# Performance work log

Measured on AMD Instinct MI355X. Metric: run time of the kernel, lower is better.

The kernel has to match this reference:

```python
import jax, jax.numpy as jnp
import numpy as np
from math import factorial

P = 3          # polynomial order
D_I = 4096     # sketch output dim per order
C = 512        # input channels
B, H, W = 8, 28, 28
GAMMA = 1e-4


def setup_inputs() -> dict:
    key = jax.random.key(0)
    k1, k2, k3 = jax.random.split(key, 3)
    x = jax.random.normal(k1, (B, H, W, C), dtype=jnp.float32)
    # AlphaInitializer: alpha_i = sqrt(exp(-2g) * (2g)^i / i!)
    gam2 = np.full(P + 1, 2.0 * GAMMA)
    numer = np.power(gam2, np.arange(P + 1))
    denom = np.array([factorial(i) for i in range(P + 1)], dtype=np.float64)
    alpha = jnp.asarray(np.sqrt(np.exp(-gam2) * numer / denom), dtype=jnp.float32)
    # count-sketch hash indices and sign bits, one pair per order t in [0, p)
    h_idx = jax.random.randint(k2, (P, C), 0, D_I)
    s_bits = jax.random.randint(k3, (P, C), 0, 2).astype(jnp.int32)
    return {"x": x, "alpha": alpha, "h_idx": h_idx, "s_bits": s_bits}


def reference(x, alpha, h_idx, s_bits):
    Bs, Hs, Ws, Ch = x.shape
    p = h_idx.shape[0]
    d_i = D_I
    signs = (2 * s_bits - 1).astype(x.dtype)          # (p, C) in {-1,+1}
    x_flat = x.reshape(-1, Ch)                        # (B*H*W, C)

    def count_sketch(h, s):
        # scatter-add channels into d_i buckets: equivalent to x_flat @ S
        return jnp.zeros((x_flat.shape[0], d_i), x.dtype).at[:, h].add(x_flat * s)

    sk = jax.vmap(count_sketch)(h_idx, signs)         # (p, N, d_i)
    xs = jnp.transpose(sk, (1, 0, 2)).reshape(Bs, Hs * Ws, p, d_i)

    xf = jnp.fft.fft(xs.astype(jnp.complex64), axis=-1)
    cp = jnp.cumprod(xf, axis=-2)[:, :, 1:, :]        # orders 2..p
    xi = jnp.real(jnp.fft.ifft(cp, axis=-1)).mean(axis=1)   # (B, p-1, d_i)

    x_p = xi * alpha[2:].reshape(1, p - 1, 1)
    zeroth = alpha[0] * jnp.ones((Bs, 1), x.dtype)
    first = alpha[1] * x.mean(axis=(1, 2))            # (B, C)
    phi = jnp.concatenate([zeroth, first, x_p.reshape(Bs, -1)], axis=-1)
    phi = jnp.sign(phi) * jnp.sqrt(jnp.abs(phi) + 1e-12)    # signed sqrt
    return phi / jnp.linalg.norm(phi, axis=-1, keepdims=True)
```

## Files before the change

kernel.cpp:

```cpp
#include <hip/hip_runtime.h>

#define BATCH 8
#define NPOS 784
#define CH 512
#define DI 4096
#define PPC 4
#define CHUNKS (NPOS / PPC)
#define PHI_LEN 8705
#define S_FLOATS (BATCH * 2 * 2049 * 2)
#define PHI_OFF S_FLOATS

__device__ __forceinline__ float2 cmul(float2 a, float2 b) {
  return make_float2(a.x * b.x - a.y * b.y, a.x * b.y + a.y * b.x);
}
__device__ __forceinline__ float2 f2add(float2 a, float2 b) {
  return make_float2(a.x + b.x, a.y + b.y);
}
__device__ __forceinline__ float2 f2sub(float2 a, float2 b) {
  return make_float2(a.x - b.x, a.y - b.y);
}

__device__ __forceinline__ void dft4(float2& a, float2& b, float2& c, float2& d) {
  float t0x = a.x + c.x, t0y = a.y + c.y;
  float t1x = a.x - c.x, t1y = a.y - c.y;
  float t2x = b.x + d.x, t2y = b.y + d.y;
  float t3x = b.x - d.x, t3y = b.y - d.y;
  a = make_float2(t0x + t2x, t0y + t2y);
  c = make_float2(t0x - t2x, t0y - t2y);
  b = make_float2(t1x + t3y, t1y - t3x);
  d = make_float2(t1x - t3y, t1y + t3x);
}

__device__ __forceinline__ void dft8(float2 v[8]) {
  float2 e0 = v[0], e1 = v[2], e2 = v[4], e3 = v[6];
  dft4(e0, e1, e2, e3);
  float2 o0 = v[1], o1 = v[3], o2 = v[5], o3 = v[7];
  dft4(o0, o1, o2, o3);
  const float r = 0.70710678118654752f;
  o1 = make_float2(r * (o1.x + o1.y), r * (o1.y - o1.x));
  o2 = make_float2(o2.y, -o2.x);
  o3 = make_float2(r * (o3.y - o3.x), -r * (o3.x + o3.y));
  v[0] = f2add(e0, o0); v[4] = f2sub(e0, o0);
  v[1] = f2add(e1, o1); v[5] = f2sub(e1, o1);
  v[2] = f2add(e2, o2); v[6] = f2sub(e2, o2);
  v[3] = f2add(e3, o3); v[7] = f2sub(e3, o3);
}

__device__ __forceinline__ void twiddle8(float2 v[8], float2 w) {
  float2 w2 = cmul(w, w);
  float2 w3 = cmul(w2, w);
  float2 w4 = cmul(w2, w2);
  v[1] = cmul(v[1], w);
  v[2] = cmul(v[2], w2);
  v[3] = cmul(v[3], w3);
  v[4] = cmul(v[4], w4);
  v[5] = cmul(v[5], cmul(w4, w));
  v[6] = cmul(v[6], cmul(w4, w2));
  v[7] = cmul(v[7], cmul(w4, w3));
}

__device__ __forceinline__ void fft_stages8(float2* Z, int t, float2 w1b,
                                            float2 w2b, float2 w3b) {
  __syncthreads();
  {
    const int base = t << 3;
    const int mask0 = (t >> 1) & 15;
    float2 v[8];
    #pragma unroll
    for (int u = 0; u < 8; ++u) v[u] = Z[(base + u) ^ mask0];
    dft8(v);
    #pragma unroll
    for (int k = 0; k < 8; ++k) Z[(base + k) ^ mask0] = v[k];
  }
  __builtin_amdgcn_wave_barrier();
  {
    const int base = ((t >> 3) << 6) + (t & 7);
    const int g4 = (t >> 3) << 2;
    float2 v[8];
    #pragma unroll
    for (int u = 0; u < 8; ++u)
      v[u] = Z[(base + (u << 3)) ^ ((g4 + (u >> 1)) & 15)];
    twiddle8(v, w1b);
    dft8(v);
    #pragma unroll
    for (int k = 0; k < 8; ++k)
      Z[(base + (k << 3)) ^ ((g4 + (k >> 1)) & 15)] = v[k];
  }
  __builtin_amdgcn_wave_barrier();
  {
    const int base = ((t >> 6) << 9) + (t & 63);
    const int jh = (t & 63) >> 4;
    float2 v[8];
    #pragma unroll
    for (int u = 0; u < 8; ++u)
      v[u] = Z[(base + (u << 6)) ^ (((u << 2) + jh) & 15)];
    twiddle8(v, w2b);
    dft8(v);
    #pragma unroll
    for (int k = 0; k < 8; ++k)
      Z[(base + (k << 6)) ^ (((k << 2) + jh) & 15)] = v[k];
  }
  __syncthreads();
  {
    const int mask3 = (t >> 4) & 15;
    float2 v[8];
    #pragma unroll
    for (int u = 0; u < 8; ++u) v[u] = Z[(t + (u << 9)) ^ mask3];
    twiddle8(v, w3b);
    dft8(v);
    #pragma unroll
    for (int k = 0; k < 8; ++k) Z[(t + (k << 9)) ^ mask3] = v[k];
  }
  __syncthreads();
}

__global__ __launch_bounds__(512) void cbp_stage1(
    const float* __restrict__ x, const float* __restrict__ alpha,
    const int* __restrict__ h_idx, const int* __restrict__ s_bits,
    float* __restrict__ ws) {
  __shared__ float2 Z[DI];
  float* Zf = (float*)Z;
  const int t = threadIdx.x;
  const int bb = blockIdx.x / CHUNKS;
  const int ch = blockIdx.x % CHUNKS;

  auto mapq = [](int h, int s) {
    int r = ((h & 7) << 9) | (((h >> 3) & 7) << 6) | (((h >> 6) & 7) << 3) |
            (h >> 9);
    return (r ^ ((r >> 4) & 15)) | ((s ^ 1) << 31);
  };
  auto sgn = [](float v, int p) {
    return __int_as_float(__float_as_int(v) ^ ((unsigned)p & 0x80000000u));
  };
  const int q0 = mapq(h_idx[t], s_bits[t]);
  const int q1 = mapq(h_idx[CH + t], s_bits[CH + t]);
  const int q2 = mapq(h_idx[2 * CH + t], s_bits[2 * CH + t]);

  float sv_, cv_;
  __sincosf(-9.8174770424681038e-2f * (float)(t & 7), &sv_, &cv_);
  const float2 w1b = make_float2(cv_, sv_);
  __sincosf(-1.2271846303085130e-2f * (float)(t & 63), &sv_, &cv_);
  const float2 w2b = make_float2(cv_, sv_);
  __sincosf(-1.5339807878856412e-3f * (float)t, &sv_, &cv_);
  const float2 w3b = make_float2(cv_, sv_);

  const int mask3 = (t >> 4) & 15;

  float2 acc2[4], acc3[4], carry[4];
  #pragma unroll
  for (int j = 0; j < 4; ++j) {
    acc2[j] = make_float2(0.f, 0.f);
    acc3[j] = make_float2(0.f, 0.f);
  }
  float acc2x = 0.f, acc3x = 0.f, carryx = 0.f;
  float xs = 0.f;

  #pragma unroll
  for (int q = 0; q < 8; ++q) Z[t + (q << 9)] = make_float2(0.f, 0.f);
  __syncthreads();

  for (int ip = 0; ip < PPC / 2; ++ip) {
    const int n0 = bb * NPOS + ch * PPC + ip * 2;
    const float xv0 = x[(size_t)n0 * CH + t];
    const float xv1 = x[(size_t)(n0 + 1) * CH + t];
    xs += xv0 + xv1;

    atomicAdd(&Zf[2 * (q0 & 0xFFF)], sgn(xv0, q0));
    atomicAdd(&Zf[2 * (q1 & 0xFFF) + 1], sgn(xv0, q1));
    fft_stages8(Z, t, w1b, w2b, w3b);
    #pragma unroll
    for (int jj = 0; jj < 4; ++jj) {
      const int k = t + (jj << 9);
      const int ak = k ^ mask3;
      const int m = (DI - k) & (DI - 1);
      const int am = m ^ ((m >> 4) & 15);
      float2 Zk = Z[ak], Zm = Z[am];
      Z[ak] = make_float2(0.f, 0.f);
      Z[am] = make_float2(0.f, 0.f);
      float2 E = make_float2(0.5f * (Zk.x + Zm.x), 0.5f * (Zk.y - Zm.y));
      float2 O = make_float2(0.5f * (Zk.y + Zm.y), -0.5f * (Zk.x - Zm.x));
      float2 P = cmul(E, O);
      carry[jj] = P;
      acc2[jj].x += P.x;
      acc2[jj].y += P.y;
    }
    if (t == 0) {
      float2 Zq = Z[2048];
      Z[2048] = make_float2(0.f, 0.f);
      carryx = Zq.x * Zq.y;
      acc2x += carryx;
    }
    __syncthreads();

    atomicAdd(&Zf[2 * (q2 & 0xFFF)], sgn(xv0, q2));
    atomicAdd(&Zf[2 * (q0 & 0xFFF) + 1], sgn(xv1, q0));
    fft_stages8(Z, t, w1b, w2b, w3b);
    #pragma unroll
    for (int jj = 0; jj < 4; ++jj) {
      const int k = t + (jj << 9);
      const int ak = k ^ mask3;
      const int m = (DI - k) & (DI - 1);
      const int am = m ^ ((m >> 4) & 15);
      float2 Zk = Z[ak], Zm = Z[am];
      Z[ak] = make_float2(0.f, 0.f);
      Z[am] = make_float2(0.f, 0.f);
      float2 E = make_float2(0.5f * (Zk.x + Zm.x), 0.5f * (Zk.y - Zm.y));
      float2 O = make_float2(0.5f * (Zk.y + Zm.y), -0.5f * (Zk.x - Zm.x));
      float2 P3 = cmul(carry[jj], E);
      acc3[jj].x += P3.x;
      acc3[jj].y += P3.y;
      carry[jj] = O;
    }
    if (t == 0) {
      float2 Zq = Z[2048];
      Z[2048] = make_float2(0.f, 0.f);
      acc3x += carryx * Zq.x;
      carryx = Zq.y;
    }
    __syncthreads();

    atomicAdd(&Zf[2 * (q1 & 0xFFF)], sgn(xv1, q1));
    atomicAdd(&Zf[2 * (q2 & 0xFFF) + 1], sgn(xv1, q2));
    fft_stages8(Z, t, w1b, w2b, w3b);
    #pragma unroll
    for (int jj = 0; jj < 4; ++jj) {
      const int k = t + (jj << 9);
      const int ak = k ^ mask3;
      const int m = (DI - k) & (DI - 1);
      const int am = m ^ ((m >> 4) & 15);
      float2 Zk = Z[ak], Zm = Z[am];
      Z[ak] = make_float2(0.f, 0.f);
      Z[am] = make_float2(0.f, 0.f);
      float2 E = make_float2(0.5f * (Zk.x + Zm.x), 0.5f * (Zk.y - Zm.y));
      float2 O = make_float2(0.5f * (Zk.y + Zm.y), -0.5f * (Zk.x - Zm.x));
      float2 P = cmul(carry[jj], E);
      acc2[jj].x += P.x;
      acc2[jj].y += P.y;
      float2 P3 = cmul(P, O);
      acc3[jj].x += P3.x;
      acc3[jj].y += P3.y;
    }
    if (t == 0) {
      float2 Zq = Z[2048];
      Z[2048] = make_float2(0.f, 0.f);
      float tt = carryx * Zq.x;
      acc2x += tt;
      acc3x += tt * Zq.y;
    }
    __syncthreads();
  }

  float* S = ws;
  #pragma unroll
  for (int jj = 0; jj < 4; ++jj) {
    const int k = t + (jj << 9);
    float* p2p = S + ((size_t)(bb * 2 + 0) * 2049 + k) * 2;
    atomicAdd(p2p, acc2[jj].x);
    atomicAdd(p2p + 1, acc2[jj].y);
    float* p3p = S + ((size_t)(bb * 2 + 1) * 2049 + k) * 2;
    atomicAdd(p3p, acc3[jj].x);
    atomicAdd(p3p + 1, acc3[jj].y);
  }
  if (t == 0) {
    atomicAdd(S + ((size_t)(bb * 2 + 0) * 2049 + 2048) * 2, acc2x);
    atomicAdd(S + ((size_t)(bb * 2 + 1) * 2049 + 2048) * 2, acc3x);
  }

  const float sc1 = alpha[1] * (1.0f / (float)NPOS);
  float* phi = ws + PHI_OFF;
  atomicAdd(&phi[(size_t)bb * PHI_LEN + 1 + t], xs * sc1);
}

__device__ inline void fft4096_r2(float2* Z, const float2* W, int tid) {
  for (int s = 1; s <= 12; ++s) {
    __syncthreads();
    const int half = 1 << (s - 1);
    const int tsh = 12 - s;
    #pragma unroll
    for (int q = 0; q < 8; ++q) {
      int bidx = tid + q * 256;
      int j = bidx & (half - 1);
      int i1 = ((bidx >> (s - 1)) << s) + j;
      int i2 = i1 + half;
      float2 w = W[j << tsh];
      float2 u = Z[i1];
      float2 v = Z[i2];
      float2 t = cmul(w, v);
      Z[i1] = make_float2(u.x + t.x, u.y + t.y);
      Z[i2] = make_float2(u.x - t.x, u.y - t.y);
    }
  }
  __syncthreads();
}

__global__ __launch_bounds__(256) void cbp_stage2(
    const float* __restrict__ ws_in, const float* __restrict__ alpha,
    float* __restrict__ ws_phi) {
  __shared__ float2 Z[DI];
  __shared__ float2 W[DI / 2];
  const int tid = threadIdx.x;

  for (int r = tid; r < DI / 2; r += 256) {
    float ang = 1.5339807878856412e-3f * (float)r;
    float sv, cv;
    sincosf(ang, &sv, &cv);
    W[r] = make_float2(cv, sv);
  }

  const int b = blockIdx.x >> 1;
  const int t = blockIdx.x & 1;
  const float* Sp = ws_in + (size_t)(b * 2 + t) * 2049 * 2;

  for (int k = tid; k <= 2048; k += 256) {
    float re = Sp[k * 2];
    float im = Sp[k * 2 + 1];
    Z[__brev((unsigned)k) >> 20] = make_float2(re, im);
    if (k > 0 && k < 2048) {
      Z[__brev((unsigned)(DI - k)) >> 20] = make_float2(re, -im);
    }
  }
  fft4096_r2(Z, W, tid);

  const float scale = alpha[2 + t] / ((float)DI * (float)NPOS);
  float* out = ws_phi + (size_t)b * PHI_LEN + 513 + t * DI;
  for (int d = tid; d < DI; d += 256) out[d] = Z[d].x * scale;
}

__global__ __launch_bounds__(256) void cbp_stage3(
    const float* __restrict__ ws_phi, const float* __restrict__ alpha,
    float* __restrict__ out) {
  __shared__ float red[4];
  const int b = blockIdx.x;
  const int tid = threadIdx.x;
  const float* pr = ws_phi + (size_t)b * PHI_LEN;
  const float a0 = alpha[0];

  float w[35];
  float ssum = 0.f;
  #pragma unroll
  for (int j = 0; j < 35; ++j) {
    const int idx = tid + j * 256;
    float wv = 0.f;
    if (idx < PHI_LEN) {
      float v = (idx == 0) ? a0 : pr[idx];
      float sq = sqrtf(fabsf(v) + 1e-12f);
      wv = (v > 0.f) ? sq : ((v < 0.f) ? -sq : 0.f);
    }
    w[j] = wv;
    ssum += wv * wv;
  }
  for (int off = 32; off > 0; off >>= 1) ssum += __shfl_down(ssum, off);
  if ((tid & 63) == 0) red[tid >> 6] = ssum;
  __syncthreads();
  const float tot = red[0] + red[1] + red[2] + red[3];
  const float inv = 1.0f / sqrtf(tot);

  #pragma unroll
  for (int j = 0; j < 35; ++j) {
    const int idx = tid + j * 256;
    if (idx < PHI_LEN) out[(size_t)b * PHI_LEN + idx] = w[j] * inv;
  }
}

extern "C" void kernel_launch(void* const* d_in, const int* in_sizes, int n_in,
                              void* d_out, int out_size, void* d_ws,
                              size_t ws_size, hipStream_t stream) {
  const float* x = (const float*)d_in[0];
  const float* alpha = (const float*)d_in[1];
  const int* h_idx = (const int*)d_in[2];
  const int* s_bits = (const int*)d_in[3];
  float* out = (float*)d_out;
  float* ws = (float*)d_ws;

  const size_t zero_bytes = (size_t)(S_FLOATS + BATCH * PHI_LEN) * sizeof(float);
  hipMemsetAsync(d_ws, 0, zero_bytes, stream);

  cbp_stage1<<<dim3(BATCH * CHUNKS), dim3(512), 0, stream>>>(x, alpha, h_idx,
                                                             s_bits, ws);
  cbp_stage2<<<dim3(BATCH * 2), dim3(256), 0, stream>>>(ws, alpha,
                                                        ws + PHI_OFF);
  cbp_stage3<<<dim3(BATCH), dim3(256), 0, stream>>>(ws + PHI_OFF, alpha, out);
}
```

Measured before the change: 224.7 us.

## Fuse last FFT stage with spectral product and replicate global accumulators

The final radix-8 FFT stage is merged with the conjugate-pair spectral product. Threads are remapped so that each k and its mirror 4096-k sit in lanes 32 apart, and the partner value is fetched with a cross-lane shuffle instead of a second shared-memory pass and barrier. Global atomic accumulation of spectra and first-order means is spread over 16 replicated buffers chosen by block index, to reduce atomic contention. Stage 2 and stage 3 then sum the replicas, which adds more memset and read traffic in exchange.

```diff
diff --git a/kernel.cpp b/kernel.cpp
--- a/kernel.cpp
+++ b/kernel.cpp
@@ -7,8 +7,14 @@
 #define PPC 4
 #define CHUNKS (NPOS / PPC)
 #define PHI_LEN 8705
-#define S_FLOATS (BATCH * 2 * 2049 * 2)
-#define PHI_OFF S_FLOATS
+#define REP 16
+#define S_STRIDE (BATCH * 2 * 2049 * 2)
+#define S_FLOATS (REP * S_STRIDE)
+#define FO_OFF S_FLOATS
+#define FO_STRIDE (BATCH * CH)
+#define FO_FLOATS (REP * FO_STRIDE)
+#define PH_OFF (FO_OFF + FO_FLOATS)
+#define ZERO_FLOATS (S_FLOATS + FO_FLOATS)
 
 __device__ __forceinline__ float2 cmul(float2 a, float2 b) {
   return make_float2(a.x * b.x - a.y * b.y, a.x * b.y + a.y * b.x);
@@ -59,59 +65,102 @@
   v[7] = cmul(v[7], cmul(w4, w3));
 }
 
-__device__ __forceinline__ void fft_stages8(float2* Z, int t, float2 w1b,
-                                            float2 w2b, float2 w3b) {
-  __syncthreads();
-  {
-    const int base = t << 3;
-    const int mask0 = (t >> 1) & 15;
-    float2 v[8];
-    #pragma unroll
-    for (int u = 0; u < 8; ++u) v[u] = Z[(base + u) ^ mask0];
-    dft8(v);
-    #pragma unroll
-    for (int k = 0; k < 8; ++k) Z[(base + k) ^ mask0] = v[k];
-  }
-  __builtin_amdgcn_wave_barrier();
-  {
-    const int base = ((t >> 3) << 6) + (t & 7);
-    const int g4 = (t >> 3) << 2;
-    float2 v[8];
-    #pragma unroll
-    for (int u = 0; u < 8; ++u)
-      v[u] = Z[(base + (u << 3)) ^ ((g4 + (u >> 1)) & 15)];
-    twiddle8(v, w1b);
-    dft8(v);
-    #pragma unroll
-    for (int k = 0; k < 8; ++k)
-      Z[(base + (k << 3)) ^ ((g4 + (k >> 1)) & 15)] = v[k];
-  }
-  __builtin_amdgcn_wave_barrier();
-  {
-    const int base = ((t >> 6) << 9) + (t & 63);
-    const int jh = (t & 63) >> 4;
-    float2 v[8];
-    #pragma unroll
-    for (int u = 0; u < 8; ++u)
-      v[u] = Z[(base + (u << 6)) ^ (((u << 2) + jh) & 15)];
-    twiddle8(v, w2b);
-    dft8(v);
-    #pragma unroll
-    for (int k = 0; k < 8; ++k)
-      Z[(base + (k << 6)) ^ (((k << 2) + jh) & 15)] = v[k];
-  }
-  __syncthreads();
-  {
-    const int mask3 = (t >> 4) & 15;
-    float2 v[8];
-    #pragma unroll
-    for (int u = 0; u < 8; ++u) v[u] = Z[(t + (u << 9)) ^ mask3];
-    twiddle8(v, w3b);
-    dft8(v);
-    #pragma unroll
-    for (int k = 0; k < 8; ++k) Z[(t + (k << 9)) ^ mask3] = v[k];
-  }
-  __syncthreads();
+template <int MODE>
+__device__ __forceinline__ void prodpair(float2 Zk, float2 Zm, float2& carry,
+                                         float2& acc2, float2& acc3) {
+  float2 E = make_float2(0.5f * (Zk.x + Zm.x), 0.5f * (Zk.y - Zm.y));
+  float2 O = make_float2(0.5f * (Zk.y + Zm.y), -0.5f * (Zk.x - Zm.x));
+  if (MODE == 0) {
+    float2 P = cmul(E, O);
+    carry = P;
+    acc2.x += P.x; acc2.y += P.y;
+  } else if (MODE == 1) {
+    float2 P3 = cmul(carry, E);
+    acc3.x += P3.x; acc3.y += P3.y;
+    carry = O;
+  } else {
+    float2 P = cmul(carry, E);
+    acc2.x += P.x; acc2.y += P.y;
+    float2 P3 = cmul(P, O);
+    acc3.x += P3.x; acc3.y += P3.y;
+  }
+}
+template <int MODE>
+__device__ __forceinline__ void nyq(float2 Zq, float& carryx, float& acc2x,
+                                    float& acc3x) {
+  if (MODE == 0) { carryx = Zq.x * Zq.y; acc2x += carryx; }
+  else if (MODE == 1) { acc3x += carryx * Zq.x; carryx = Zq.y; }
+  else { float tt = carryx * Zq.x; acc2x += tt; acc3x += tt * Zq.y; }
+}
+
+__device__ __forceinline__ void s0w(float2* Z, int t) {
+  const int base = t << 3;
+  const int m0 = (t >> 1) & 15;
+  float2 v[8];
+  #pragma unroll
+  for (int u = 0; u < 8; ++u) v[u] = Z[(base + u) ^ m0];
+  dft8(v);
+  #pragma unroll
+  for (int k = 0; k < 8; ++k) Z[(base + k) ^ m0] = v[k];
+}
+__device__ __forceinline__ void s1w(float2* Z, int t, float2 w) {
+  const int base = ((t >> 3) << 6) + (t & 7);
+  const int g4 = (t >> 3) << 2;
+  float2 v[8];
+  #pragma unroll
+  for (int u = 0; u < 8; ++u)
+    v[u] = Z[(base + (u << 3)) ^ ((g4 + (u >> 1)) & 15)];
+  twiddle8(v, w);
+  dft8(v);
+  #pragma unroll
+  for (int k = 0; k < 8; ++k)
+    Z[(base + (k << 3)) ^ ((g4 + (k >> 1)) & 15)] = v[k];
+}
+__device__ __forceinline__ void s2w(float2* Z, int t, float2 w) {
+  const int base = ((t >> 6) << 9) + (t & 63);
+  const int jh = (t & 63) >> 4;
+  float2 v[8];
+  #pragma unroll
+  for (int u = 0; u < 8; ++u)
+    v[u] = Z[(base + (u << 6)) ^ (((u << 2) + jh) & 15)];
+  twiddle8(v, w);
+  dft8(v);
+  #pragma unroll
+  for (int k = 0; k < 8; ++k)
+    Z[(base + (k << 6)) ^ (((k << 2) + jh) & 15)] = v[k];
+}
+
+template <int MODE>
+__device__ __forceinline__ void s3prod(float2* Z, int g, float2 wG,
+                                       bool selfp, float2 carry[4],
+                                       float2 acc2[4], float2 acc3[4],
+                                       float& carryx, float& acc2x,
+                                       float& acc3x) {
+  const int mg = (g >> 4) & 15;
+  float2 v[8];
+  #pragma unroll
+  for (int u = 0; u < 8; ++u) v[u] = Z[(g + (u << 9)) ^ mg];
+  #pragma unroll
+  for (int u = 0; u < 8; ++u) Z[(g + (u << 9)) ^ mg] = make_float2(0.f, 0.f);
+  twiddle8(v, wG);
+  dft8(v);
+  float2 pv[4];
+  #pragma unroll
+  for (int r = 0; r < 4; ++r) {
+    pv[r].x = __shfl_xor(v[7 - r].x, 32);
+    pv[r].y = __shfl_xor(v[7 - r].y, 32);
+  }
+  if (selfp) {
+    if (g == 0) {
+      pv[0] = v[0]; pv[1] = v[7]; pv[2] = v[6]; pv[3] = v[5];
+    } else {
+      pv[0] = v[7]; pv[1] = v[6]; pv[2] = v[5]; pv[3] = v[4];
+    }
+  }
+  #pragma unroll
+  for (int r = 0; r < 4; ++r)
+    prodpair<MODE>(v[r], pv[r], carry[r], acc2[r], acc3[r]);
+  if (g == 0) nyq<MODE>(v[4], carryx, acc2x, acc3x);
 }
 
 __global__ __launch_bounds__(512) void cbp_stage1(
@@ -121,8 +170,16 @@
   __shared__ float2 Z[DI];
   float* Zf = (float*)Z;
   const int t = threadIdx.x;
+  const int w = t >> 6, l = t & 63;
   const int bb = blockIdx.x / CHUNKS;
   const int ch = blockIdx.x % CHUNKS;
+  const int rep = blockIdx.x & (REP - 1);
+
+  int g;
+  if (l < 32) g = 32 * w + l;
+  else if (w == 0 && l == 32) g = 256;
+  else g = 544 - 32 * w - l;
+  const bool selfp = (w == 0) && ((l & 31) == 0);
 
   auto mapq = [](int h, int s) {
     int r = ((h & 7) << 9) | (((h >> 3) & 7) << 6) | (((h >> 6) & 7) << 3) |
@@ -141,10 +198,8 @@
   const float2 w1b = make_float2(cv_, sv_);
   __sincosf(-1.2271846303085130e-2f * (float)(t & 63), &sv_, &cv_);
   const float2 w2b = make_float2(cv_, sv_);
-  __sincosf(-1.5339807878856412e-3f * (float)t, &sv_, &cv_);
-  const float2 w3b = make_float2(cv_, sv_);
-
-  const int mask3 = (t >> 4) & 15;
+  __sincosf(-1.5339807878856412e-3f * (float)g, &sv_, &cv_);
+  const float2 wG = make_float2(cv_, sv_);
 
   float2 acc2[4], acc3[4], carry[4];
   #pragma unroll
@@ -167,108 +222,59 @@
 
     atomicAdd(&Zf[2 * (q0 & 0xFFF)], sgn(xv0, q0));
     atomicAdd(&Zf[2 * (q1 & 0xFFF) + 1], sgn(xv0, q1));
-    fft_stages8(Z, t, w1b, w2b, w3b);
-    #pragma unroll
-    for (int jj = 0; jj < 4; ++jj) {
-      const int k = t + (jj << 9);
-      const int ak = k ^ mask3;
-      const int m = (DI - k) & (DI - 1);
-      const int am = m ^ ((m >> 4) & 15);
-      float2 Zk = Z[ak], Zm = Z[am];
-      Z[ak] = make_float2(0.f, 0.f);
-      Z[am] = make_float2(0.f, 0.f);
-      float2 E = make_float2(0.5f * (Zk.x + Zm.x), 0.5f * (Zk.y - Zm.y));
-      float2 O = make_float2(0.5f * (Zk.y + Zm.y), -0.5f * (Zk.x - Zm.x));
-      float2 P = cmul(E, O);
-      carry[jj] = P;
-      acc2[jj].x += P.x;
-      acc2[jj].y += P.y;
-    }
-    if (t == 0) {
-      float2 Zq = Z[2048];
-      Z[2048] = make_float2(0.f, 0.f);
-      carryx = Zq.x * Zq.y;
-      acc2x += carryx;
-    }
+    __syncthreads();
+    s0w(Z, t);
+    __builtin_amdgcn_wave_barrier();
+    s1w(Z, t, w1b);
+    __builtin_amdgcn_wave_barrier();
+    s2w(Z, t, w2b);
+    __syncthreads();
+    s3prod<0>(Z, g, wG, selfp, carry, acc2, acc3, carryx, acc2x, acc3x);
     __syncthreads();
 
     atomicAdd(&Zf[2 * (q2 & 0xFFF)], sgn(xv0, q2));
     atomicAdd(&Zf[2 * (q0 & 0xFFF) + 1], sgn(xv1, q0));
-    fft_stages8(Z, t, w1b, w2b, w3b);
-    #pragma unroll
-    for (int jj = 0; jj < 4; ++jj) {
-      const int k = t + (jj << 9);
-      const int ak = k ^ mask3;
-      const int m = (DI - k) & (DI - 1);
-      const int am = m ^ ((m >> 4) & 15);
-      float2 Zk = Z[ak], Zm = Z[am];
-      Z[ak] = make_float2(0.f, 0.f);
-      Z[am] = make_float2(0.f, 0.f);
-      float2 E = make_float2(0.5f * (Zk.x + Zm.x), 0.5f * (Zk.y - Zm.y));
-      float2 O = make_float2(0.5f * (Zk.y + Zm.y), -0.5f * (Zk.x - Zm.x));
-      float2 P3 = cmul(carry[jj], E);
-      acc3[jj].x += P3.x;
-      acc3[jj].y += P3.y;
-      carry[jj] = O;
-    }
-    if (t == 0) {
-      float2 Zq = Z[2048];
-      Z[2048] = make_float2(0.f, 0.f);
-      acc3x += carryx * Zq.x;
-      carryx = Zq.y;
-    }
+    __syncthreads();
+    s0w(Z, t);
+    __builtin_amdgcn_wave_barrier();
+    s1w(Z, t, w1b);
+    __builtin_amdgcn_wave_barrier();
+    s2w(Z, t, w2b);
+    __syncthreads();
+    s3prod<1>(Z, g, wG, selfp, carry, acc2, acc3, carryx, acc2x, acc3x);
     __syncthreads();
 
     atomicAdd(&Zf[2 * (q1 & 0xFFF)], sgn(xv1, q1));
     atomicAdd(&Zf[2 * (q2 & 0xFFF) + 1], sgn(xv1, q2));
-    fft_stages8(Z, t, w1b, w2b, w3b);
-    #pragma unroll
-    for (int jj = 0; jj < 4; ++jj) {
-      const int k = t + (jj << 9);
-      const int ak = k ^ mask3;
-      const int m = (DI - k) & (DI - 1);
-      const int am = m ^ ((m >> 4) & 15);
-      float2 Zk = Z[ak], Zm = Z[am];
-      Z[ak] = make_float2(0.f, 0.f);
-      Z[am] = make_float2(0.f, 0.f);
-      float2 E = make_float2(0.5f * (Zk.x + Zm.x), 0.5f * (Zk.y - Zm.y));
-      float2 O = make_float2(0.5f * (Zk.y + Zm.y), -0.5f * (Zk.x - Zm.x));
-      float2 P = cmul(carry[jj], E);
-      acc2[jj].x += P.x;
-      acc2[jj].y += P.y;
-      float2 P3 = cmul(P, O);
-      acc3[jj].x += P3.x;
-      acc3[jj].y += P3.y;
-    }
-    if (t == 0) {
-      float2 Zq = Z[2048];
-      Z[2048] = make_float2(0.f, 0.f);
-      float tt = carryx * Zq.x;
-      acc2x += tt;
-      acc3x += tt * Zq.y;
-    }
-    __syncthreads();
-  }
-
-  float* S = ws;
-  #pragma unroll
-  for (int jj = 0; jj < 4; ++jj) {
-    const int k = t + (jj << 9);
+    __syncthreads();
+    s0w(Z, t);
+    __builtin_amdgcn_wave_barrier();
+    s1w(Z, t, w1b);
+    __builtin_amdgcn_wave_barrier();
+    s2w(Z, t, w2b);
+    __syncthreads();
+    s3prod<2>(Z, g, wG, selfp, carry, acc2, acc3, carryx, acc2x, acc3x);
+    __syncthreads();
+  }
+
+  float* S = ws + (size_t)rep * S_STRIDE;
+  #pragma unroll
+  for (int r = 0; r < 4; ++r) {
+    const int k = g + (r << 9);
     float* p2p = S + ((size_t)(bb * 2 + 0) * 2049 + k) * 2;
-    atomicAdd(p2p, acc2[jj].x);
-    atomicAdd(p2p + 1, acc2[jj].y);
+    atomicAdd(p2p, acc2[r].x);
+    atomicAdd(p2p + 1, acc2[r].y);
     float* p3p = S + ((size_t)(bb * 2 + 1) * 2049 + k) * 2;
-    atomicAdd(p3p, acc3[jj].x);
-    atomicAdd(p3p + 1, acc3[jj].y);
-  }
-  if (t == 0) {
+    atomicAdd(p3p, acc3[r].x);
+    atomicAdd(p3p + 1, acc3[r].y);
+  }
+  if (g == 0) {
     atomicAdd(S + ((size_t)(bb * 2 + 0) * 2049 + 2048) * 2, acc2x);
     atomicAdd(S + ((size_t)(bb * 2 + 1) * 2049 + 2048) * 2, acc3x);
   }
 
   const float sc1 = alpha[1] * (1.0f / (float)NPOS);
-  float* phi = ws + PHI_OFF;
-  atomicAdd(&phi[(size_t)bb * PHI_LEN + 1 + t], xs * sc1);
+  atomicAdd(&ws[FO_OFF + (size_t)rep * FO_STRIDE + bb * CH + t], xs * sc1);
 }
 
 __device__ inline void fft4096_r2(float2* Z, const float2* W, int tid) {
@@ -295,7 +301,7 @@
 
 __global__ __launch_bounds__(256) void cbp_stage2(
     const float* __restrict__ ws_in, const float* __restrict__ alpha,
-    float* __restrict__ ws_phi) {
+    float* __restrict__ ws_out) {
   __shared__ float2 Z[DI];
   __shared__ float2 W[DI / 2];
   const int tid = threadIdx.x;
@@ -309,11 +315,15 @@
 
   const int b = blockIdx.x >> 1;
   const int t = blockIdx.x & 1;
-  const float* Sp = ws_in + (size_t)(b * 2 + t) * 2049 * 2;
+  const float* Sp = ws_in + ((size_t)(b * 2 + t) * 2049) * 2;
 
   for (int k = tid; k <= 2048; k += 256) {
-    float re = Sp[k * 2];
-    float im = Sp[k * 2 + 1];
+    float re = 0.f, im = 0.f;
+    #pragma unroll
+    for (int rp = 0; rp < REP; ++rp) {
+      re += Sp[(size_t)rp * S_STRIDE + k * 2];
+      im += Sp[(size_t)rp * S_STRIDE + k * 2 + 1];
+    }
     Z[__brev((unsigned)k) >> 20] = make_float2(re, im);
     if (k > 0 && k < 2048) {
       Z[__brev((unsigned)(DI - k)) >> 20] = make_float2(re, -im);
@@ -322,17 +332,16 @@
   fft4096_r2(Z, W, tid);
 
   const float scale = alpha[2 + t] / ((float)DI * (float)NPOS);
-  float* out = ws_phi + (size_t)b * PHI_LEN + 513 + t * DI;
+  float* out = ws_out + PH_OFF + (size_t)(b * 2 + t) * DI;
   for (int d = tid; d < DI; d += 256) out[d] = Z[d].x * scale;
 }
 
 __global__ __launch_bounds__(256) void cbp_stage3(
-    const float* __restrict__ ws_phi, const float* __restrict__ alpha,
+    const float* __restrict__ ws_in, const float* __restrict__ alpha,
     float* __restrict__ out) {
   __shared__ float red[4];
   const int b = blockIdx.x;
   const int tid = threadIdx.x;
-  const float* pr = ws_phi + (size_t)b * PHI_LEN;
   const float a0 = alpha[0];
 
   float w[35];
@@ -342,7 +351,17 @@
     const int idx = tid + j * 256;
     float wv = 0.f;
     if (idx < PHI_LEN) {
-      float v = (idx == 0) ? a0 : pr[idx];
+      float v;
+      if (idx == 0) {
+        v = a0;
+      } else if (idx <= 512) {
+        v = 0.f;
+        #pragma unroll
+        for (int rp = 0; rp < REP; ++rp)
+          v += ws_in[FO_OFF + (size_t)rp * FO_STRIDE + b * CH + (idx - 1)];
+      } else {
+        v = ws_in[PH_OFF + (size_t)b * 2 * DI + (idx - 513)];
+      }
       float sq = sqrtf(fabsf(v) + 1e-12f);
       wv = (v > 0.f) ? sq : ((v < 0.f) ? -sq : 0.f);
     }
@@ -372,12 +391,10 @@
   float* out = (float*)d_out;
   float* ws = (float*)d_ws;
 
-  const size_t zero_bytes = (size_t)(S_FLOATS + BATCH * PHI_LEN) * sizeof(float);
-  hipMemsetAsync(d_ws, 0, zero_bytes, stream);
+  hipMemsetAsync(d_ws, 0, (size_t)ZERO_FLOATS * sizeof(float), stream);
 
   cbp_stage1<<<dim3(BATCH * CHUNKS), dim3(512), 0, stream>>>(x, alpha, h_idx,
                                                              s_bits, ws);
-  cbp_stage2<<<dim3(BATCH * 2), dim3(256), 0, stream>>>(ws, alpha,
-                                                        ws + PHI_OFF);
-  cbp_stage3<<<dim3(BATCH), dim3(256), 0, stream>>>(ws + PHI_OFF, alpha, out);
-}
+  cbp_stage2<<<dim3(BATCH * 2), dim3(256), 0, stream>>>(ws, alpha, ws);
+  cbp_stage3<<<dim3(BATCH), dim3(256), 0, stream>>>(ws, alpha, out);
+}
```

Result: slower. 236.7 us (+5.4%).
